# Optimization experiments

Measured on AMD Instinct MI355X. Metric: run time of the kernel, lower is better.

## Reference

```python
import jax, jax.numpy as jnp
import numpy as np

N_NODES = 50000
N_EDGES = 800000
N_REL = 4
F_IN = 128
H1 = 64          # RGCN out
HEADS = 4
D_H = 32         # per-head GAT out
N_GRAPHS = 64


def setup_inputs() -> dict:
    key = jax.random.key(0)
    ks = jax.random.split(key, 16)
    inp = {
        "x": jax.random.normal(ks[0], (N_NODES, F_IN), dtype=jnp.float32),
        "edge_index": jax.random.randint(ks[1], (2, N_EDGES), 0, N_NODES, dtype=jnp.int32),
        "edge_type": jax.random.randint(ks[2], (N_EDGES,), 0, N_REL, dtype=jnp.int32),
        "batch": jnp.sort(jax.random.randint(ks[3], (N_NODES,), 0, N_GRAPHS, dtype=jnp.int32)),
        # RGCNConv params (relation weights, root weight, bias)
        "W_rel": jax.random.normal(ks[4], (N_REL, F_IN, H1), dtype=jnp.float32) * 0.05,
        "W_root": jax.random.normal(ks[5], (F_IN, H1), dtype=jnp.float32) * 0.05,
        "b_rgcn": jnp.zeros((H1,), dtype=jnp.float32),
        # GATConv params
        "W_gat": jax.random.normal(ks[6], (H1, HEADS * D_H), dtype=jnp.float32) * 0.1,
        "att_src": jax.random.normal(ks[7], (HEADS, D_H), dtype=jnp.float32) * 0.1,
        "att_dst": jax.random.normal(ks[8], (HEADS, D_H), dtype=jnp.float32) * 0.1,
        "b_gat": jnp.zeros((HEADS * D_H,), dtype=jnp.float32),
        # dense layers
        "W1": jax.random.normal(ks[9], (HEADS * D_H, 16), dtype=jnp.float32) * 0.05,
        "b1": jnp.zeros((16,), dtype=jnp.float32),
        "W2": jax.random.normal(ks[10], (16, 1), dtype=jnp.float32) * 0.2,
        "b2": jnp.zeros((1,), dtype=jnp.float32),
    }
    return inp


def reference(x, W_rel, W_root, b_rgcn, W_gat, att_src, att_dst, b_gat,
              W1, b1, W2, b2, edge_index, edge_type, batch):
    src, dst = edge_index[0], edge_index[1]
    n = x.shape[0]

    # ---- RGCNConv: mean aggregation per relation, then linear (linearity lets
    # us aggregate raw features first, then apply W_rel) + root transform ----
    xs = x[src]                                            # [E, F_IN]
    out = x @ W_root + b_rgcn                              # [N, H1]
    for r in range(N_REL):
        mask = (edge_type == r).astype(x.dtype)            # [E]
        s = jax.ops.segment_sum(xs * mask[:, None], dst, num_segments=n)
        cnt = jax.ops.segment_sum(mask, dst, num_segments=n)
        mean_r = s / jnp.maximum(cnt, 1.0)[:, None]        # [N, F_IN]
        out = out + mean_r @ W_rel[r]
    h = jax.nn.relu(out)                                   # [N, H1]
    # (dropout omitted: deterministic/eval reference)

    # ---- GATConv (heads=4, concat, no self loops, edge_attr unused) ----
    g = (h @ W_gat).reshape(n, HEADS, D_H)                 # [N, H, D]
    a_s = jnp.einsum('nhd,hd->nh', g, att_src)             # [N, H]
    a_d = jnp.einsum('nhd,hd->nh', g, att_dst)
    e = jax.nn.leaky_relu(a_s[src] + a_d[dst], 0.2)        # [E, H]
    m = jax.ops.segment_max(e, dst, num_segments=n)        # [N, H]
    ex = jnp.exp(e - m[dst])                               # [E, H]
    den = jax.ops.segment_sum(ex, dst, num_segments=n)     # [N, H]
    alpha = ex / den[dst]
    o = jax.ops.segment_sum(alpha[:, :, None] * g[src], dst, num_segments=n)
    o = o.reshape(n, HEADS * D_H) + b_gat                  # [N, 128]
    o = jax.nn.leaky_relu(o, 0.01)

    # ---- dense1 -> leaky_relu -> global max pool -> dense2 ----
    z = jax.nn.leaky_relu(o @ W1 + b1, 0.01)               # [N, 16]
    p = jax.ops.segment_max(z, batch, num_segments=N_GRAPHS)  # [G, 16]
    y = p @ W2 + b2                                        # [G, 1]
    return y
```

## Files before the change

kernel.cpp:

```cpp
#include <hip/hip_runtime.h>
#include <hip/hip_bf16.h>

constexpr int N_NODES = 50000;
constexpr int N_EDGES = 800000;
constexpr int F_IN = 128;
constexpr int H1 = 64;
constexpr int HEADS = 4;
constexpr int D_H = 32;
constexpr int HOUT = HEADS * D_H;
constexpr int N_REL = 4;
constexpr int N_GRAPHS = 64;
constexpr int MBIG = H1 * (1 + N_REL);
constexpr int NBLK = (N_NODES + 255) / 256;
constexpr int N_PAD = 50048;

typedef __attribute__((ext_vector_type(8))) short bf16x8;
typedef __attribute__((ext_vector_type(4))) float f32x4;

__device__ __forceinline__ unsigned f2mono(float f) {
  unsigned u = __float_as_uint(f);
  return (u & 0x80000000u) ? ~u : (u | 0x80000000u);
}
__device__ __forceinline__ float mono2f(unsigned m) {
  unsigned u = (m & 0x80000000u) ? (m & 0x7FFFFFFFu) : ~m;
  return __uint_as_float(u);
}
constexpr unsigned MONO_NEG_INF = 0x007FFFFFu;

__device__ __forceinline__ unsigned short f2bf(float f) {
  unsigned u = __float_as_uint(f);
  unsigned r = (u + 0x7FFFu + ((u >> 16) & 1u)) >> 16;
  return (unsigned short)r;
}
__device__ __forceinline__ float bf2f(unsigned short h) {
  return __uint_as_float((unsigned)h << 16);
}
__device__ __forceinline__ float bflo(unsigned u) { return __uint_as_float(u << 16); }
__device__ __forceinline__ float bfhi(unsigned u) { return __uint_as_float(u & 0xFFFF0000u); }

constexpr int HIST_BLOCKS = (N_EDGES + 255) / 256;
constexpr int WT_BLOCKS = (MBIG * F_IN + HOUT * H1 + 255) / 256;

__global__ __launch_bounds__(256) void pre_fused(
    const float* __restrict__ W_root, const float* __restrict__ W_rel,
    const float* __restrict__ W_gat,
    const float* __restrict__ att_src, const float* __restrict__ att_dst,
    const int* __restrict__ dst,
    unsigned short* __restrict__ WbT_hi, unsigned short* __restrict__ WbT_lo,
    unsigned short* __restrict__ WgT_hi, unsigned short* __restrict__ WgT_lo,
    int* __restrict__ deg, int* __restrict__ rank,
    unsigned* __restrict__ pm,
    float* __restrict__ was, float* __restrict__ wad) {
  int b = blockIdx.x;
  if (b < HIST_BLOCKS) {
    int e = b * 256 + threadIdx.x;
    if (e < N_EDGES) rank[e] = atomicAdd(&deg[dst[e]], 1);
  } else if (b < HIST_BLOCKS + WT_BLOCKS) {
    int i = (b - HIST_BLOCKS) * 256 + threadIdx.x;
    if (i < MBIG * F_IN) {
      int c = i / F_IN, k = i % F_IN;
      float w = (c < H1) ? W_root[k * H1 + c]
                         : W_rel[((size_t)(((c - H1) >> 6) * F_IN + k)) * H1 + ((c - H1) & 63)];
      unsigned short hi = f2bf(w);
      WbT_hi[i] = hi;
      WbT_lo[i] = f2bf(w - bf2f(hi));
    } else {
      int j = i - MBIG * F_IN;
      if (j < HOUT * H1) {
        int c = j / H1, k = j % H1;
        float w = W_gat[k * HOUT + c];
        unsigned short hi = f2bf(w);
        WgT_hi[j] = hi;
        WgT_lo[j] = f2bf(w - bf2f(hi));
      }
    }
  } else if (b == HIST_BLOCKS + WT_BLOCKS) {
    for (int i = threadIdx.x; i < N_GRAPHS * 16; i += 256) pm[i] = MONO_NEG_INF;
  } else {
    int t = threadIdx.x;
    int k = t >> 2, hh = t & 3;
    float s = 0.f, d2 = 0.f;
#pragma unroll 8
    for (int dd = 0; dd < D_H; ++dd) {
      float wg = W_gat[k * HOUT + hh * D_H + dd];
      s += wg * att_src[hh * D_H + dd];
      d2 += wg * att_dst[hh * D_H + dd];
    }
    was[t] = s;
    wad[t] = d2;
  }
}

template <int K, bool SPLIT>
__device__ __forceinline__ void gemm_body(int bx, int by,
    const void* __restrict__ A0,
    const void* __restrict__ A1,
    const unsigned short* __restrict__ BT_hi,
    const unsigned short* __restrict__ BT_lo,
    unsigned short* __restrict__ Cbf, int N, int M) {
  __shared__ unsigned short Ah[64 * K];
  __shared__ unsigned short Al[64 * K];
  const int tid = threadIdx.x;
  const int rowBase = bx * 64;
  const int colBase = by * 64;
  if (SPLIT) {
    const unsigned short* Ahi_ = (const unsigned short*)A0;
    const unsigned short* Alo_ = (const unsigned short*)A1;
    constexpr int KQ8 = K / 8;
    for (int s = tid; s < 64 * KQ8; s += 256) {
      int r = s / KQ8, c8 = (s % KQ8) * 8;
      size_t gi = (size_t)(rowBase + r) * K + c8;
      int sw = c8 ^ ((r & 7) << 3);
      *reinterpret_cast<uint4*>(&Ah[r * K + sw]) =
          *reinterpret_cast<const uint4*>(&Ahi_[gi]);
      *reinterpret_cast<uint4*>(&Al[r * K + sw]) =
          *reinterpret_cast<const uint4*>(&Alo_[gi]);
    }
  } else {
    const float* Af = (const float*)A0;
    constexpr int KQ4 = K / 4;
    for (int s = tid; s < 64 * KQ4; s += 256) {
      int r = s / KQ4, c4 = (s % KQ4) * 4;
      int gr = rowBase + r;
      float4 v = make_float4(0.f, 0.f, 0.f, 0.f);
      if (gr < N) v = *reinterpret_cast<const float4*>(&Af[(size_t)gr * K + c4]);
      ushort4 hi, lo;
      hi.x = f2bf(v.x); lo.x = f2bf(v.x - bf2f(hi.x));
      hi.y = f2bf(v.y); lo.y = f2bf(v.y - bf2f(hi.y));
      hi.z = f2bf(v.z); lo.z = f2bf(v.z - bf2f(hi.z));
      hi.w = f2bf(v.w); lo.w = f2bf(v.w - bf2f(hi.w));
      int sw = c4 ^ ((r & 7) << 3);
      *reinterpret_cast<ushort4*>(&Ah[r * K + sw]) = hi;
      *reinterpret_cast<ushort4*>(&Al[r * K + sw]) = lo;
    }
  }
  __syncthreads();
  const int wv = tid >> 6, lane = tid & 63;
  const int wr = (wv >> 1) * 32, wc = (wv & 1) * 32;
  const int lrow = lane & 15, lkc = lane >> 4;
  f32x4 acc[2][2] = {};
#pragma unroll
  for (int ks = 0; ks < K; ks += 32) {
    bf16x8 ah[2], al[2], bh[2], bl[2];
#pragma unroll
    for (int fr = 0; fr < 2; ++fr) {
      int r = wr + fr * 16 + lrow;
      int sw = (ks + lkc * 8) ^ ((r & 7) << 3);
      ah[fr] = *reinterpret_cast<const bf16x8*>(&Ah[r * K + sw]);
      al[fr] = *reinterpret_cast<const bf16x8*>(&Al[r * K + sw]);
    }
#pragma unroll
    for (int fc = 0; fc < 2; ++fc) {
      int c = colBase + wc + fc * 16 + lrow;
      bh[fc] = *reinterpret_cast<const bf16x8*>(&BT_hi[(size_t)c * K + ks + lkc * 8]);
      bl[fc] = *reinterpret_cast<const bf16x8*>(&BT_lo[(size_t)c * K + ks + lkc * 8]);
    }
#pragma unroll
    for (int fr = 0; fr < 2; ++fr)
#pragma unroll
      for (int fc = 0; fc < 2; ++fc) {
        acc[fr][fc] = __builtin_amdgcn_mfma_f32_16x16x32_bf16(ah[fr], bh[fc], acc[fr][fc], 0, 0, 0);
        acc[fr][fc] = __builtin_amdgcn_mfma_f32_16x16x32_bf16(ah[fr], bl[fc], acc[fr][fc], 0, 0, 0);
        acc[fr][fc] = __builtin_amdgcn_mfma_f32_16x16x32_bf16(al[fr], bh[fc], acc[fr][fc], 0, 0, 0);
      }
  }
#pragma unroll
  for (int fr = 0; fr < 2; ++fr) {
#pragma unroll
    for (int i = 0; i < 4; ++i) {
      int row = rowBase + wr + fr * 16 + lkc * 4 + i;
      if (row < N) {
#pragma unroll
        for (int fc = 0; fc < 2; ++fc) {
          int col = colBase + wc + fc * 16 + lrow;
          Cbf[(size_t)row * M + col] = f2bf(acc[fr][fc][i]);
        }
      }
    }
  }
}

constexpr int G1_BX = N_PAD / 64;
constexpr int G1_BLOCKS = G1_BX * (MBIG / 64);
__global__ __launch_bounds__(256) void gemm1_fill(
    const float* __restrict__ x,
    const unsigned short* __restrict__ wbt_hi, const unsigned short* __restrict__ wbt_lo,
    unsigned short* __restrict__ xtbf,
    const int* __restrict__ src, const int* __restrict__ dst,
    const int* __restrict__ etype, const int* __restrict__ off,
    const int* __restrict__ rank, int* __restrict__ eprep) {
  if (blockIdx.x < G1_BLOCKS) {
    gemm_body<128, false>(blockIdx.x % G1_BX, blockIdx.x / G1_BX,
                          x, nullptr, wbt_hi, wbt_lo, xtbf, N_NODES, MBIG);
  } else {
    int e = (blockIdx.x - G1_BLOCKS) * 256 + threadIdx.x;
    if (e < N_EDGES) {
      int pos = off[dst[e]] + rank[e];
      eprep[pos] = src[e] | (etype[e] << 16);
    }
  }
}

__global__ __launch_bounds__(256) void gemm2_k(
    const unsigned short* __restrict__ hhi, const unsigned short* __restrict__ hlo,
    const unsigned short* __restrict__ wgt_hi, const unsigned short* __restrict__ wgt_lo,
    unsigned short* __restrict__ gbf) {
  gemm_body<64, true>(blockIdx.x % G1_BX, blockIdx.x / G1_BX,
                      hhi, hlo, wgt_hi, wgt_lo, gbf, N_NODES, HOUT);
}

__global__ __launch_bounds__(256) void k_s1(const int* __restrict__ deg,
                                            int* __restrict__ bsum) {
  __shared__ int ss[256];
  int t = threadIdx.x;
  int i = blockIdx.x * 256 + t;
  ss[t] = (i < N_NODES) ? deg[i] : 0;
  __syncthreads();
  for (int d = 128; d > 0; d >>= 1) {
    if (t < d) ss[t] += ss[t + d];
    __syncthreads();
  }
  if (t == 0) bsum[blockIdx.x] = ss[0];
}

__global__ __launch_bounds__(256) void k_s2(const int* __restrict__ bsum,
                                            int* __restrict__ bbase,
                                            int* __restrict__ off) {
  __shared__ int ss[256];
  int t = threadIdx.x;
  int v = (t < NBLK) ? bsum[t] : 0;
  ss[t] = v;
  __syncthreads();
  for (int d = 1; d < 256; d <<= 1) {
    int u = (t >= d) ? ss[t - d] : 0;
    __syncthreads();
    ss[t] += u;
    __syncthreads();
  }
  if (t < NBLK) bbase[t] = ss[t] - v;
  if (t == NBLK - 1) off[N_NODES] = ss[t];
}

__global__ __launch_bounds__(256) void k_s3(const int* __restrict__ deg,
                                            const int* __restrict__ bbase,
                                            int* __restrict__ off) {
  __shared__ int ss[256];
  int t = threadIdx.x;
  int i = blockIdx.x * 256 + t;
  int v = (i < N_NODES) ? deg[i] : 0;
  ss[t] = v;
  __syncthreads();
  for (int d = 1; d < 256; d <<= 1) {
    int u = (t >= d) ? ss[t - d] : 0;
    __syncthreads();
    ss[t] += u;
    __syncthreads();
  }
  if (i < N_NODES) off[i] = bbase[blockIdx.x] + ss[t] - v;
}

__global__ __launch_bounds__(256) void rgcn_gather(const unsigned short* __restrict__ xtbf,
                                                   const int* __restrict__ off,
                                                   const int* __restrict__ eprep,
                                                   const float* __restrict__ b_rgcn,
                                                   const float* __restrict__ was,
                                                   const float* __restrict__ wad,
                                                   unsigned short* __restrict__ hhi,
                                                   unsigned short* __restrict__ hlo,
                                                   float* __restrict__ a_s,
                                                   float* __restrict__ a_d) {
  int wid = (blockIdx.x * 256 + threadIdx.x) >> 6;
  int lane = threadIdx.x & 63;
  int half = lane >> 5;
  int cp = lane & 31;
  int start = off[wid], end = off[wid + 1];
  float a0x=0.f,a0y=0.f,a1x=0.f,a1y=0.f,a2x=0.f,a2y=0.f,a3x=0.f,a3y=0.f;
  int c0=0,c1=0,c2=0,c3=0;
  int niter = (end - start + 1) >> 1;
  for (int t = 0; t < niter; t += 2) {
    int idx0 = start + 2 * t + half;
    int idx1 = idx0 + 2;
    int p0 = (idx0 < end) ? eprep[idx0] : 0x70000;
    int p1 = (idx1 < end) ? eprep[idx1] : 0x70000;
    int s0 = p0 & 0xFFFF, r0 = p0 >> 16;
    int s1 = p1 & 0xFFFF, r1 = p1 >> 16;
    unsigned u0 = *reinterpret_cast<const unsigned*>(
        &xtbf[(size_t)s0 * MBIG + H1 + (r0 << 6) + cp * 2]);
    unsigned u1 = *reinterpret_cast<const unsigned*>(
        &xtbf[(size_t)s1 * MBIG + H1 + (r1 << 6) + cp * 2]);
    float v0x = bflo(u0), v0y = bfhi(u0);
    float v1x = bflo(u1), v1y = bfhi(u1);
    a0x += (r0==0)?v0x:0.f; a0y += (r0==0)?v0y:0.f; c0 += (r0==0);
    a1x += (r0==1)?v0x:0.f; a1y += (r0==1)?v0y:0.f; c1 += (r0==1);
    a2x += (r0==2)?v0x:0.f; a2y += (r0==2)?v0y:0.f; c2 += (r0==2);
    a3x += (r0==3)?v0x:0.f; a3y += (r0==3)?v0y:0.f; c3 += (r0==3);
    a0x += (r1==0)?v1x:0.f; a0y += (r1==0)?v1y:0.f; c0 += (r1==0);
    a1x += (r1==1)?v1x:0.f; a1y += (r1==1)?v1y:0.f; c1 += (r1==1);
    a2x += (r1==2)?v1x:0.f; a2y += (r1==2)?v1y:0.f; c2 += (r1==2);
    a3x += (r1==3)?v1x:0.f; a3y += (r1==3)?v1y:0.f; c3 += (r1==3);
  }
  a0x += __shfl_xor(a0x, 32); a0y += __shfl_xor(a0y, 32);
  a1x += __shfl_xor(a1x, 32); a1y += __shfl_xor(a1y, 32);
  a2x += __shfl_xor(a2x, 32); a2y += __shfl_xor(a2y, 32);
  a3x += __shfl_xor(a3x, 32); a3y += __shfl_xor(a3y, 32);
  c0 += __shfl_xor(c0, 32); c1 += __shfl_xor(c1, 32);
  c2 += __shfl_xor(c2, 32); c3 += __shfl_xor(c3, 32);
  if (half == 0) {
    unsigned ur = *reinterpret_cast<const unsigned*>(&xtbf[(size_t)wid * MBIG + cp * 2]);
    float2 bb = *reinterpret_cast<const float2*>(&b_rgcn[cp * 2]);
    float i0 = 1.0f / (float)max(c0, 1);
    float i1 = 1.0f / (float)max(c1, 1);
    float i2 = 1.0f / (float)max(c2, 1);
    float i3 = 1.0f / (float)max(c3, 1);
    float vx = bflo(ur) + bb.x + a0x * i0 + a1x * i1 + a2x * i2 + a3x * i3;
    float vy = bfhi(ur) + bb.y + a0y * i0 + a1y * i1 + a2y * i2 + a3y * i3;
    vx = fmaxf(vx, 0.f);
    vy = fmaxf(vy, 0.f);
    unsigned short hx = f2bf(vx), hy = f2bf(vy);
    ushort2 hv = {hx, hy};
    ushort2 lv = {f2bf(vx - bf2f(hx)), f2bf(vy - bf2f(hy))};
    *reinterpret_cast<ushort2*>(&hhi[(size_t)wid * H1 + cp * 2]) = hv;
    *reinterpret_cast<ushort2*>(&hlo[(size_t)wid * H1 + cp * 2]) = lv;
    float4 wsA = *reinterpret_cast<const float4*>(&was[cp * 8]);
    float4 wsB = *reinterpret_cast<const float4*>(&was[cp * 8 + 4]);
    float4 wdA = *reinterpret_cast<const float4*>(&wad[cp * 8]);
    float4 wdB = *reinterpret_cast<const float4*>(&wad[cp * 8 + 4]);
    float ps0 = vx * wsA.x + vy * wsB.x;
    float ps1 = vx * wsA.y + vy * wsB.y;
    float ps2 = vx * wsA.z + vy * wsB.z;
    float ps3 = vx * wsA.w + vy * wsB.w;
    float pd0 = vx * wdA.x + vy * wdB.x;
    float pd1 = vx * wdA.y + vy * wdB.y;
    float pd2 = vx * wdA.z + vy * wdB.z;
    float pd3 = vx * wdA.w + vy * wdB.w;
#pragma unroll
    for (int d = 1; d < 32; d <<= 1) {
      ps0 += __shfl_xor(ps0, d); ps1 += __shfl_xor(ps1, d);
      ps2 += __shfl_xor(ps2, d); ps3 += __shfl_xor(ps3, d);
      pd0 += __shfl_xor(pd0, d); pd1 += __shfl_xor(pd1, d);
      pd2 += __shfl_xor(pd2, d); pd3 += __shfl_xor(pd3, d);
    }
    if (cp == 0) {
      *reinterpret_cast<float4*>(&a_s[(size_t)wid * 4]) = make_float4(ps0, ps1, ps2, ps3);
      *reinterpret_cast<float4*>(&a_d[(size_t)wid * 4]) = make_float4(pd0, pd1, pd2, pd3);
    }
  }
}

constexpr int GAT_BLOCKS = 2048;
constexpr int GAT_WAVES = GAT_BLOCKS * 4;
__global__ __launch_bounds__(256) void gat_fused(const unsigned short* __restrict__ gbf,
                                                 const float* __restrict__ a_s,
                                                 const float* __restrict__ a_d,
                                                 const int* __restrict__ off,
                                                 const int* __restrict__ eprep,
                                                 const float* __restrict__ b_gat,
                                                 const float* __restrict__ W1,
                                                 const float* __restrict__ b1,
                                                 const int* __restrict__ batch,
                                                 unsigned* __restrict__ p_mono) {
  __shared__ float w1s[HOUT * 16];
  __shared__ float ob[4][HOUT];
  __shared__ unsigned sp[N_GRAPHS * 16];
  const int t = threadIdx.x;
  for (int i = t; i < HOUT * 16; i += 256) w1s[i] = W1[i];
  for (int i = t; i < N_GRAPHS * 16; i += 256) sp[i] = MONO_NEG_INF;
  __syncthreads();
  const int wv = t >> 6, lane = t & 63;
  const int hh = lane >> 4;
  const int jj = lane & 15, grp = lane >> 4;
  const int w = blockIdx.x * 4 + wv;
  const int q = N_NODES / GAT_WAVES;
  const int r = N_NODES % GAT_WAVES;
  const int nbeg = w * q + ((w < r) ? w : r);
  const int ncnt = q + ((w < r) ? 1 : 0);
  for (int wid = nbeg; wid < nbeg + ncnt; ++wid) {
    int start = off[wid], end = off[wid + 1];
    float4 ad4 = *reinterpret_cast<const float4*>(a_d + (size_t)wid * 4);
    float adh = (hh == 0) ? ad4.x : (hh == 1) ? ad4.y : (hh == 2) ? ad4.z : ad4.w;
    float ox = 0.f, oy = 0.f, den = 0.f;
    int i = start;
    for (; i + 4 <= end; i += 4) {
      int p0 = eprep[i], p1 = eprep[i + 1], p2 = eprep[i + 2], p3 = eprep[i + 3];
      int s0 = p0 & 0xFFFF, s1 = p1 & 0xFFFF, s2 = p2 & 0xFFFF, s3 = p3 & 0xFFFF;
      float as0 = a_s[(size_t)s0 * 4 + hh];
      float as1 = a_s[(size_t)s1 * 4 + hh];
      float as2 = a_s[(size_t)s2 * 4 + hh];
      float as3 = a_s[(size_t)s3 * 4 + hh];
      unsigned u0 = *reinterpret_cast<const unsigned*>(&gbf[(size_t)s0 * HOUT + lane * 2]);
      unsigned u1 = *reinterpret_cast<const unsigned*>(&gbf[(size_t)s1 * HOUT + lane * 2]);
      unsigned u2 = *reinterpret_cast<const unsigned*>(&gbf[(size_t)s2 * HOUT + lane * 2]);
      unsigned u3 = *reinterpret_cast<const unsigned*>(&gbf[(size_t)s3 * HOUT + lane * 2]);
      float e0 = as0 + adh; e0 = (e0 > 0.f) ? e0 : 0.2f * e0;
      float e1 = as1 + adh; e1 = (e1 > 0.f) ? e1 : 0.2f * e1;
      float e2 = as2 + adh; e2 = (e2 > 0.f) ? e2 : 0.2f * e2;
      float e3 = as3 + adh; e3 = (e3 > 0.f) ? e3 : 0.2f * e3;
      float x0 = __expf(e0), x1 = __expf(e1), x2 = __expf(e2), x3 = __expf(e3);
      den += x0 + x1 + x2 + x3;
      ox += x0 * bflo(u0) + x1 * bflo(u1) + x2 * bflo(u2) + x3 * bflo(u3);
      oy += x0 * bfhi(u0) + x1 * bfhi(u1) + x2 * bfhi(u2) + x3 * bfhi(u3);
    }
    for (; i < end; ++i) {
      int p = eprep[i];
      int s = p & 0xFFFF;
      float as = a_s[(size_t)s * 4 + hh];
      unsigned u = *reinterpret_cast<const unsigned*>(&gbf[(size_t)s * HOUT + lane * 2]);
      float e = as + adh; e = (e > 0.f) ? e : 0.2f * e;
      float ex = __expf(e);
      den += ex;
      ox += ex * bflo(u);
      oy += ex * bfhi(u);
    }
    float dinv = (den > 0.f) ? (1.0f / den) : 0.f;
    float2 bg = *reinterpret_cast<const float2*>(b_gat + lane * 2);
    float vx = ox * dinv + bg.x; vx = (vx > 0.f) ? vx : 0.01f * vx;
    float vy = oy * dinv + bg.y; vy = (vy > 0.f) ? vy : 0.01f * vy;
    *reinterpret_cast<float2*>(&ob[wv][lane * 2]) = make_float2(vx, vy);
    float acc = 0.f;
#pragma unroll 8
    for (int i2 = 0; i2 < 32; ++i2) {
      int c = grp + 4 * i2;
      acc += ob[wv][c] * w1s[c * 16 + jj];
    }
    acc += __shfl_xor(acc, 16);
    acc += __shfl_xor(acc, 32);
    float z = acc + b1[jj];
    z = (z > 0.f) ? z : 0.01f * z;
    int b = batch[wid];
    if (lane < 16) atomicMax(&sp[b * 16 + jj], f2mono(z));
  }
  __syncthreads();
  for (int i = t; i < N_GRAPHS * 16; i += 256) {
    unsigned v = sp[i];
    if (v != MONO_NEG_INF) atomicMax(p_mono + i, v);
  }
}

__global__ void final_y(const unsigned* __restrict__ p_mono,
                        const float* __restrict__ W2,
                        const float* __restrict__ b2,
                        float* __restrict__ y) {
  int gr = threadIdx.x;
  if (gr >= N_GRAPHS) return;
  float acc = b2[0];
#pragma unroll
  for (int k = 0; k < 16; ++k) acc += mono2f(p_mono[gr * 16 + k]) * W2[k];
  y[gr] = acc;
}

extern "C" void kernel_launch(void* const* d_in, const int* in_sizes, int n_in,
                              void* d_out, int out_size, void* d_ws, size_t ws_size,
                              hipStream_t stream) {
  const float* x       = (const float*)d_in[0];
  const int*   eidx    = (const int*)d_in[1];
  const int*   etype   = (const int*)d_in[2];
  const int*   batch   = (const int*)d_in[3];
  const float* W_rel   = (const float*)d_in[4];
  const float* W_root  = (const float*)d_in[5];
  const float* b_rgcn  = (const float*)d_in[6];
  const float* W_gat   = (const float*)d_in[7];
  const float* att_src = (const float*)d_in[8];
  const float* att_dst = (const float*)d_in[9];
  const float* b_gat   = (const float*)d_in[10];
  const float* W1      = (const float*)d_in[11];
  const float* b1      = (const float*)d_in[12];
  const float* W2      = (const float*)d_in[13];
  const float* b2      = (const float*)d_in[14];
  float* y = (float*)d_out;

  const int* src = eidx;
  const int* dst = eidx + N_EDGES;

  float* ws = (float*)d_ws;
  const size_t OFF_XTBF= 0;
  const size_t OFF_GBF = 0;
  const size_t OFF_HHI = 8007680;
  const size_t OFF_HLO = 9609216;
  const size_t OFF_AS  = 11210752;
  const size_t OFF_AD  = 11410752;
  const size_t OFF_PM  = 11610752;
  const size_t OFF_DEG = 11611776;
  const size_t OFF_OFFS= 11661776;
  const size_t OFF_RANK= 11711780;
  const size_t OFF_EP  = 12511780;
  const size_t OFF_BS  = 13311780;
  const size_t OFF_BB  = 13311976;
  const size_t OFF_WAS = 13312176;
  const size_t OFF_WAD = 13312432;
  const size_t OFF_WBH = 13312688;
  const size_t OFF_WBL = 13333168;
  const size_t OFF_WGH = 13353648;
  const size_t OFF_WGL = 13357744;
  const size_t TOTAL_F = 13361840;
  if (ws_size < TOTAL_F * sizeof(float)) return;

  unsigned short* xtbf = (unsigned short*)(ws + OFF_XTBF);
  unsigned short* gbf  = (unsigned short*)(ws + OFF_GBF);
  unsigned short* hhi  = (unsigned short*)(ws + OFF_HHI);
  unsigned short* hlo  = (unsigned short*)(ws + OFF_HLO);
  float* a_s   = ws + OFF_AS;
  float* a_d   = ws + OFF_AD;
  unsigned* pm = (unsigned*)(ws + OFF_PM);
  int* deg     = (int*)(ws + OFF_DEG);
  int* offs    = (int*)(ws + OFF_OFFS);
  int* rank    = (int*)(ws + OFF_RANK);
  int* eprep   = (int*)(ws + OFF_EP);
  int* bsum    = (int*)(ws + OFF_BS);
  int* bbase   = (int*)(ws + OFF_BB);
  float* was   = ws + OFF_WAS;
  float* wad   = ws + OFF_WAD;
  unsigned short* wbt_hi = (unsigned short*)(ws + OFF_WBH);
  unsigned short* wbt_lo = (unsigned short*)(ws + OFF_WBL);
  unsigned short* wgt_hi = (unsigned short*)(ws + OFF_WGH);
  unsigned short* wgt_lo = (unsigned short*)(ws + OFF_WGL);

  hipMemsetAsync(deg, 0, N_NODES * sizeof(int), stream);

  pre_fused<<<HIST_BLOCKS + WT_BLOCKS + 2, 256, 0, stream>>>(
      W_root, W_rel, W_gat, att_src, att_dst, dst,
      wbt_hi, wbt_lo, wgt_hi, wgt_lo, deg, rank, pm, was, wad);

  k_s1<<<NBLK, 256, 0, stream>>>(deg, bsum);
  k_s2<<<1, 256, 0, stream>>>(bsum, bbase, offs);
  k_s3<<<NBLK, 256, 0, stream>>>(deg, bbase, offs);

  gemm1_fill<<<G1_BLOCKS + HIST_BLOCKS, 256, 0, stream>>>(
      x, wbt_hi, wbt_lo, xtbf, src, dst, etype, offs, rank, eprep);

  rgcn_gather<<<N_NODES / 4, 256, 0, stream>>>(xtbf, offs, eprep, b_rgcn,
                                               was, wad, hhi, hlo, a_s, a_d);

  gemm2_k<<<G1_BX * (HOUT / 64), 256, 0, stream>>>(hhi, hlo, wgt_hi, wgt_lo, gbf);

  gat_fused<<<GAT_BLOCKS, 256, 0, stream>>>(gbf, a_s, a_d, offs, eprep, b_gat,
                                            W1, b1, batch, pm);

  final_y<<<1, 64, 0, stream>>>(pm, W2, b2, y);
}
```

Before: 214.1 us.

## Split gemm1 K into two LDS chunks with prefetch and grouped block order

The K=128 GEMM is rewritten to stage A in two 64-wide LDS chunks, which halves shared memory per block, and the second chunk's global loads are issued before the first chunk's MFMA work so they overlap. Blocks are remapped so that groups of 8 row-tiles cover all 5 column tiles together, which improves L2 reuse of the x rows. The grid is padded to 3920 blocks and blocks with an out-of-range bx exit early. The cost is an extra barrier and extra registers held for the prefetched data.

```diff
diff --git a/kernel.cpp b/kernel.cpp
--- a/kernel.cpp
+++ b/kernel.cpp
@@ -91,48 +91,131 @@
   }
 }
 
-template <int K, bool SPLIT>
-__device__ __forceinline__ void gemm_body(int bx, int by,
-    const void* __restrict__ A0,
-    const void* __restrict__ A1,
+__device__ __forceinline__ void gemm_body128(int bx, int by,
+    const float* __restrict__ Af,
     const unsigned short* __restrict__ BT_hi,
     const unsigned short* __restrict__ BT_lo,
     unsigned short* __restrict__ Cbf, int N, int M) {
+  constexpr int K = 128, KC = 64;
+  __shared__ unsigned short Ah[64 * KC];
+  __shared__ unsigned short Al[64 * KC];
+  const int tid = threadIdx.x;
+  const int rowBase = bx * 64;
+  const int colBase = by * 64;
+  const int wv = tid >> 6, lane = tid & 63;
+  const int wr = (wv >> 1) * 32, wc = (wv & 1) * 32;
+  const int lrow = lane & 15, lkc = lane >> 4;
+  int r_[4], c4_[4];
+#pragma unroll
+  for (int it = 0; it < 4; ++it) {
+    int s = it * 256 + tid;
+    r_[it] = s >> 4;
+    c4_[it] = (s & 15) * 4;
+  }
+  f32x4 acc[2][2] = {};
+#pragma unroll
+  for (int it = 0; it < 4; ++it) {
+    int gr = rowBase + r_[it];
+    float4 v = make_float4(0.f, 0.f, 0.f, 0.f);
+    if (gr < N) v = *reinterpret_cast<const float4*>(&Af[(size_t)gr * K + c4_[it]]);
+    ushort4 hi, lo;
+    hi.x = f2bf(v.x); lo.x = f2bf(v.x - bf2f(hi.x));
+    hi.y = f2bf(v.y); lo.y = f2bf(v.y - bf2f(hi.y));
+    hi.z = f2bf(v.z); lo.z = f2bf(v.z - bf2f(hi.z));
+    hi.w = f2bf(v.w); lo.w = f2bf(v.w - bf2f(hi.w));
+    int sw = c4_[it] ^ ((r_[it] & 7) << 3);
+    *reinterpret_cast<ushort4*>(&Ah[r_[it] * KC + sw]) = hi;
+    *reinterpret_cast<ushort4*>(&Al[r_[it] * KC + sw]) = lo;
+  }
+  __syncthreads();
+  float4 v1[4];
+#pragma unroll
+  for (int it = 0; it < 4; ++it) {
+    int gr = rowBase + r_[it];
+    v1[it] = make_float4(0.f, 0.f, 0.f, 0.f);
+    if (gr < N) v1[it] = *reinterpret_cast<const float4*>(&Af[(size_t)gr * K + KC + c4_[it]]);
+  }
+#pragma unroll
+  for (int ch = 0; ch < 2; ++ch) {
+    if (ch == 1) {
+      __syncthreads();
+#pragma unroll
+      for (int it = 0; it < 4; ++it) {
+        float4 v = v1[it];
+        ushort4 hi, lo;
+        hi.x = f2bf(v.x); lo.x = f2bf(v.x - bf2f(hi.x));
+        hi.y = f2bf(v.y); lo.y = f2bf(v.y - bf2f(hi.y));
+        hi.z = f2bf(v.z); lo.z = f2bf(v.z - bf2f(hi.z));
+        hi.w = f2bf(v.w); lo.w = f2bf(v.w - bf2f(hi.w));
+        int sw = c4_[it] ^ ((r_[it] & 7) << 3);
+        *reinterpret_cast<ushort4*>(&Ah[r_[it] * KC + sw]) = hi;
+        *reinterpret_cast<ushort4*>(&Al[r_[it] * KC + sw]) = lo;
+      }
+      __syncthreads();
+    }
+#pragma unroll
+    for (int ks = 0; ks < KC; ks += 32) {
+      bf16x8 ah[2], al[2], bh[2], bl[2];
+#pragma unroll
+      for (int fr = 0; fr < 2; ++fr) {
+        int r = wr + fr * 16 + lrow;
+        int sw = (ks + lkc * 8) ^ ((r & 7) << 3);
+        ah[fr] = *reinterpret_cast<const bf16x8*>(&Ah[r * KC + sw]);
+        al[fr] = *reinterpret_cast<const bf16x8*>(&Al[r * KC + sw]);
+      }
+#pragma unroll
+      for (int fc = 0; fc < 2; ++fc) {
+        int c = colBase + wc + fc * 16 + lrow;
+        bh[fc] = *reinterpret_cast<const bf16x8*>(&BT_hi[(size_t)c * K + ch * KC + ks + lkc * 8]);
+        bl[fc] = *reinterpret_cast<const bf16x8*>(&BT_lo[(size_t)c * K + ch * KC + ks + lkc * 8]);
+      }
+#pragma unroll
+      for (int fr = 0; fr < 2; ++fr)
+#pragma unroll
+        for (int fc = 0; fc < 2; ++fc) {
+          acc[fr][fc] = __builtin_amdgcn_mfma_f32_16x16x32_bf16(ah[fr], bh[fc], acc[fr][fc], 0, 0, 0);
+          acc[fr][fc] = __builtin_amdgcn_mfma_f32_16x16x32_bf16(ah[fr], bl[fc], acc[fr][fc], 0, 0, 0);
+          acc[fr][fc] = __builtin_amdgcn_mfma_f32_16x16x32_bf16(al[fr], bh[fc], acc[fr][fc], 0, 0, 0);
+        }
+    }
+  }
+#pragma unroll
+  for (int fr = 0; fr < 2; ++fr) {
+#pragma unroll
+    for (int i = 0; i < 4; ++i) {
+      int row = rowBase + wr + fr * 16 + lkc * 4 + i;
+      if (row < N) {
+#pragma unroll
+        for (int fc = 0; fc < 2; ++fc) {
+          int col = colBase + wc + fc * 16 + lrow;
+          Cbf[(size_t)row * M + col] = f2bf(acc[fr][fc][i]);
+        }
+      }
+    }
+  }
+}
+
+__device__ __forceinline__ void gemm_body64(int bx, int by,
+    const unsigned short* __restrict__ Ahi_,
+    const unsigned short* __restrict__ Alo_,
+    const unsigned short* __restrict__ BT_hi,
+    const unsigned short* __restrict__ BT_lo,
+    unsigned short* __restrict__ Cbf, int N, int M) {
+  constexpr int K = 64;
   __shared__ unsigned short Ah[64 * K];
   __shared__ unsigned short Al[64 * K];
   const int tid = threadIdx.x;
   const int rowBase = bx * 64;
   const int colBase = by * 64;
-  if (SPLIT) {
-    const unsigned short* Ahi_ = (const unsigned short*)A0;
-    const unsigned short* Alo_ = (const unsigned short*)A1;
-    constexpr int KQ8 = K / 8;
-    for (int s = tid; s < 64 * KQ8; s += 256) {
-      int r = s / KQ8, c8 = (s % KQ8) * 8;
-      size_t gi = (size_t)(rowBase + r) * K + c8;
-      int sw = c8 ^ ((r & 7) << 3);
-      *reinterpret_cast<uint4*>(&Ah[r * K + sw]) =
-          *reinterpret_cast<const uint4*>(&Ahi_[gi]);
-      *reinterpret_cast<uint4*>(&Al[r * K + sw]) =
-          *reinterpret_cast<const uint4*>(&Alo_[gi]);
-    }
-  } else {
-    const float* Af = (const float*)A0;
-    constexpr int KQ4 = K / 4;
-    for (int s = tid; s < 64 * KQ4; s += 256) {
-      int r = s / KQ4, c4 = (s % KQ4) * 4;
-      int gr = rowBase + r;
-      float4 v = make_float4(0.f, 0.f, 0.f, 0.f);
-      if (gr < N) v = *reinterpret_cast<const float4*>(&Af[(size_t)gr * K + c4]);
-      ushort4 hi, lo;
-      hi.x = f2bf(v.x); lo.x = f2bf(v.x - bf2f(hi.x));
-      hi.y = f2bf(v.y); lo.y = f2bf(v.y - bf2f(hi.y));
-      hi.z = f2bf(v.z); lo.z = f2bf(v.z - bf2f(hi.z));
-      hi.w = f2bf(v.w); lo.w = f2bf(v.w - bf2f(hi.w));
-      int sw = c4 ^ ((r & 7) << 3);
-      *reinterpret_cast<ushort4*>(&Ah[r * K + sw]) = hi;
-      *reinterpret_cast<ushort4*>(&Al[r * K + sw]) = lo;
-    }
+  constexpr int KQ8 = K / 8;
+  for (int s = tid; s < 64 * KQ8; s += 256) {
+    int r = s / KQ8, c8 = (s % KQ8) * 8;
+    size_t gi = (size_t)(rowBase + r) * K + c8;
+    int sw = c8 ^ ((r & 7) << 3);
+    *reinterpret_cast<uint4*>(&Ah[r * K + sw]) =
+        *reinterpret_cast<const uint4*>(&Ahi_[gi]);
+    *reinterpret_cast<uint4*>(&Al[r * K + sw]) =
+        *reinterpret_cast<const uint4*>(&Alo_[gi]);
   }
   __syncthreads();
   const int wv = tid >> 6, lane = tid & 63;
@@ -181,7 +264,7 @@
 }
 
 constexpr int G1_BX = N_PAD / 64;
-constexpr int G1_BLOCKS = G1_BX * (MBIG / 64);
+constexpr int G1_GRID = 3920;
 __global__ __launch_bounds__(256) void gemm1_fill(
     const float* __restrict__ x,
     const unsigned short* __restrict__ wbt_hi, const unsigned short* __restrict__ wbt_lo,
@@ -189,11 +272,15 @@
     const int* __restrict__ src, const int* __restrict__ dst,
     const int* __restrict__ etype, const int* __restrict__ off,
     const int* __restrict__ rank, int* __restrict__ eprep) {
-  if (blockIdx.x < G1_BLOCKS) {
-    gemm_body<128, false>(blockIdx.x % G1_BX, blockIdx.x / G1_BX,
-                          x, nullptr, wbt_hi, wbt_lo, xtbf, N_NODES, MBIG);
+  if (blockIdx.x < G1_GRID) {
+    int b = blockIdx.x;
+    int r8 = b & 7, s = b >> 3;
+    int by = s % 5, q = s / 5;
+    int bx = q * 8 + r8;
+    if (bx < G1_BX)
+      gemm_body128(bx, by, x, wbt_hi, wbt_lo, xtbf, N_NODES, MBIG);
   } else {
-    int e = (blockIdx.x - G1_BLOCKS) * 256 + threadIdx.x;
+    int e = (blockIdx.x - G1_GRID) * 256 + threadIdx.x;
     if (e < N_EDGES) {
       int pos = off[dst[e]] + rank[e];
       eprep[pos] = src[e] | (etype[e] << 16);
@@ -205,8 +292,8 @@
     const unsigned short* __restrict__ hhi, const unsigned short* __restrict__ hlo,
     const unsigned short* __restrict__ wgt_hi, const unsigned short* __restrict__ wgt_lo,
     unsigned short* __restrict__ gbf) {
-  gemm_body<64, true>(blockIdx.x % G1_BX, blockIdx.x / G1_BX,
-                      hhi, hlo, wgt_hi, wgt_lo, gbf, N_NODES, HOUT);
+  gemm_body64(blockIdx.x % G1_BX, blockIdx.x / G1_BX,
+              hhi, hlo, wgt_hi, wgt_lo, gbf, N_NODES, HOUT);
 }
 
 __global__ __launch_bounds__(256) void k_s1(const int* __restrict__ deg,
@@ -524,7 +611,7 @@
   k_s2<<<1, 256, 0, stream>>>(bsum, bbase, offs);
   k_s3<<<NBLK, 256, 0, stream>>>(deg, bbase, offs);
 
-  gemm1_fill<<<G1_BLOCKS + HIST_BLOCKS, 256, 0, stream>>>(
+  gemm1_fill<<<G1_GRID + HIST_BLOCKS, 256, 0, stream>>>(
       x, wbt_hi, wbt_lo, xtbf, src, dst, etype, offs, rank, eprep);
 
   rgcn_gather<<<N_NODES / 4, 256, 0, stream>>>(xtbf, offs, eprep, b_rgcn,
```

After: 208.0 us, median of 2. 2.8% less time.
